# Optimization experiments

Measured on AMD Instinct MI355X. Metric: run time of the kernel, lower is better.

Reference implementation:

```python
import jax, jax.numpy as jnp
import numpy as np

EMBED_DIM = 1024
NUM_HEADS = 16
HEAD_DIM = EMBED_DIM // NUM_HEADS
SCALE = HEAD_DIM ** -0.5


def setup_inputs() -> dict:
    key = jax.random.key(0)
    k_x, k_qkv_w, k_qkv_b, k_p_w, k_p_b = jax.random.split(key, 5)
    B, N, C = 4, 2048, EMBED_DIM
    std = C ** -0.5
    return {
        "x": jax.random.normal(k_x, (B, N, C), dtype=jnp.float32),
        "qkv_w": jax.random.normal(k_qkv_w, (C, 3 * C), dtype=jnp.float32) * std,
        "qkv_b": jax.random.normal(k_qkv_b, (3 * C,), dtype=jnp.float32) * 0.02,
        "proj_w": jax.random.normal(k_p_w, (C, C), dtype=jnp.float32) * std,
        "proj_b": jax.random.normal(k_p_b, (C,), dtype=jnp.float32) * 0.02,
    }


def reference(x, qkv_w, qkv_b, proj_w, proj_b):
    B, N, C = x.shape
    H, D = NUM_HEADS, HEAD_DIM
    # fused QKV projection: [B, N, 3C] -> [3, B, H, N, D]
    qkv = (x @ qkv_w + qkv_b).reshape(B, N, 3, H, D).transpose(2, 0, 3, 1, 4)
    q, k, v = qkv[0], qkv[1], qkv[2]
    # explicit N x N attention (faithful to the original, no fused SDPA)
    attn = jnp.einsum("bhqd,bhkd->bhqk", q, k) * SCALE
    attn = jax.nn.softmax(attn, axis=-1)
    out = jnp.einsum("bhqk,bhkd->bhqd", attn, v)  # [B, H, N, D]
    out = out.transpose(0, 2, 1, 3).reshape(B, N, C)
    return out @ proj_w + proj_b
```

## Files before the change

kernel.cpp:

```cpp
#include <hip/hip_runtime.h>
#include <hip/hip_bf16.h>

typedef __bf16 bf16x8 __attribute__((ext_vector_type(8)));
typedef __bf16 bf16x4 __attribute__((ext_vector_type(4)));
typedef float  f32x4  __attribute__((ext_vector_type(4)));

#define MFMA_BF16(a, b, c) __builtin_amdgcn_mfma_f32_16x16x32_bf16((a), (b), (c), 0, 0, 0)

typedef const __attribute__((address_space(1))) void* gas_ptr;
typedef __attribute__((address_space(3))) void* las_ptr;

__device__ __forceinline__ void gload_lds16(const void* g, void* l) {
    __builtin_amdgcn_global_load_lds((gas_ptr)g, (las_ptr)l, 16, 0, 0);
}

__device__ __forceinline__ float fast_exp2(float x) {
#if __has_builtin(__builtin_amdgcn_exp2f)
    return __builtin_amdgcn_exp2f(x);
#else
    return __builtin_exp2f(x);
#endif
}

#define LOG2E 1.44269504088896f
#define QSCALE 0.1803368801111204f

__global__ __launch_bounds__(256) void prep_fused(const float* __restrict__ x,
                                                  const float* __restrict__ qkv_w,
                                                  const float* __restrict__ proj_w,
                                                  __bf16* __restrict__ Xb,
                                                  __bf16* __restrict__ Wqkvt,
                                                  __bf16* __restrict__ Wpt) {
    const int b = blockIdx.x;
    if (b < 8192) {
        int i = b * 256 + threadIdx.x;
        float4 v = ((const float4*)x)[i];
        bf16x4 o = {(__bf16)v.x, (__bf16)v.y, (__bf16)v.z, (__bf16)v.w};
        ((bf16x4*)Xb)[i] = o;
        return;
    }
    __shared__ float t[32][33];
    const float* in;
    __bf16* out;
    int R, C, bx, by;
    if (b < 11264) {
        int bb = b - 8192;
        in = qkv_w; out = Wqkvt; R = 1024; C = 3072;
        bx = (bb % 96) * 32; by = (bb / 96) * 32;
    } else {
        int bb = b - 11264;
        in = proj_w; out = Wpt; R = 1024; C = 1024;
        bx = (bb % 32) * 32; by = (bb / 32) * 32;
    }
    const int tx = threadIdx.x & 31, ty = threadIdx.x >> 5;
    int xcol = bx + tx;
    for (int j = ty; j < 32; j += 8)
        t[j][tx] = in[(size_t)(by + j) * C + xcol];
    __syncthreads();
    int x2 = by + tx;
    for (int j = ty; j < 32; j += 8)
        out[(size_t)(bx + j) * R + x2] = (__bf16)t[tx][j];
}

template <int MODE>
__global__ __launch_bounds__(256) void gemm_bt(const __bf16* __restrict__ A,
                                               const __bf16* __restrict__ Bt,
                                               const float* __restrict__ bias,
                                               float* __restrict__ outp,
                                               __bf16* __restrict__ Qp,
                                               __bf16* __restrict__ Kp,
                                               __bf16* __restrict__ Vp,
                                               int M, int Nn, int K) {
    __shared__ __align__(16) __bf16 SA[3][4096];
    __shared__ __align__(16) __bf16 SB[3][4096];
    const int tid = threadIdx.x, lane = tid & 63, w = tid >> 6;
    const int wr = w >> 1, wc = w & 1;
    const int nbx = Nn >> 7;
    const int nwg = (M >> 7) * nbx;
    const int cpx = nwg >> 3;
    const int id = blockIdx.x;
    const int nid = (id & 7) * cpx + (id >> 3);
    const int row0 = (nid / nbx) * 128, col0 = (nid % nbx) * 128;
    const __bf16* Ag = A + (size_t)row0 * K;
    const __bf16* Bg = Bt + (size_t)col0 * K;
    const int lr = lane >> 2;
    const int srcc = ((lane & 3) ^ ((lane >> 3) & 3)) * 8;
    const int frow = lane & 15, fq = lane >> 4;
    const int rdoff = (fq ^ ((frow >> 1) & 3)) * 8;
    f32x4 acc[4][4];
    for (int i = 0; i < 4; ++i)
        for (int j = 0; j < 4; ++j) acc[i][j] = (f32x4)0.f;

    auto stage = [&](int t, __bf16* Ad, __bf16* Bd) {
#pragma unroll
        for (int it = 0; it < 2; ++it) {
            int ci = 2 * w + it;
            gload_lds16(Ag + (size_t)(ci * 16 + lr) * K + t * 32 + srcc, Ad + ci * 512);
            gload_lds16(Bg + (size_t)(ci * 16 + lr) * K + t * 32 + srcc, Bd + ci * 512);
        }
    };

    const int NK = K >> 5;
    __bf16 *cA = SA[0], *cB = SB[0];
    __bf16 *nA = SA[1], *nB = SB[1];
    __bf16 *sA = SA[2], *sB = SB[2];
    stage(0, cA, cB);
    stage(1, nA, nB);

    for (int t = 0; t < NK; ++t) {
        if (t < NK - 1)
            asm volatile("s_waitcnt vmcnt(4)" ::: "memory");
        else
            asm volatile("s_waitcnt vmcnt(0)" ::: "memory");
        __builtin_amdgcn_s_barrier();
        if (t + 2 < NK) stage(t + 2, sA, sB);

        bf16x8 af[4], bf[4];
#pragma unroll
        for (int i = 0; i < 4; ++i)
            af[i] = *(const bf16x8*)&cA[(wr * 64 + i * 16 + frow) * 32 + rdoff];
#pragma unroll
        for (int j = 0; j < 4; ++j)
            bf[j] = *(const bf16x8*)&cB[(wc * 64 + j * 16 + frow) * 32 + rdoff];
#pragma unroll
        for (int i = 0; i < 4; ++i)
#pragma unroll
            for (int j = 0; j < 4; ++j) acc[i][j] = MFMA_BF16(af[i], bf[j], acc[i][j]);

        __bf16* tA = cA; cA = nA; nA = sA; sA = tA;
        __bf16* tB = cB; cB = nB; nB = sB; sB = tB;
    }

    for (int i = 0; i < 4; ++i) {
        int rbase = row0 + wr * 64 + i * 16 + fq * 4;
        for (int j = 0; j < 4; ++j) {
            int c = col0 + wc * 64 + j * 16 + frow;
            float bv = bias[c];
            if (MODE == 0) {
                int which = c >> 10;
                int h = (c >> 6) & 15;
                int d = c & 63;
                if (which == 2) {
                    int b = rbase >> 11, n = rbase & 2047;
                    int nph = (n & ~31) | (((n >> 2) & 3) << 3) | (((n >> 4) & 1) << 2) |
                              (n & 3);
                    bf16x4 vv = {(__bf16)(acc[i][j][0] + bv), (__bf16)(acc[i][j][1] + bv),
                                 (__bf16)(acc[i][j][2] + bv), (__bf16)(acc[i][j][3] + bv)};
                    *(bf16x4*)&Vp[(size_t)(((b << 4) + h) * 64 + d) * 2048 + nph] = vv;
                } else {
                    for (int rg = 0; rg < 4; ++rg) {
                        int rr = rbase + rg;
                        int b = rr >> 11, n = rr & 2047;
                        float v = acc[i][j][rg] + bv;
                        if (which == 0)
                            Qp[(size_t)(((b << 4) + h) * 2048 + n) * 64 + d] =
                                (__bf16)(v * QSCALE);
                        else
                            Kp[(size_t)(((b << 4) + h) * 2048 + n) * 64 + d] = (__bf16)v;
                    }
                }
            } else {
                for (int rg = 0; rg < 4; ++rg)
                    outp[(size_t)(rbase + rg) * Nn + c] = acc[i][j][rg] + bv;
            }
        }
    }
}

__global__ __launch_bounds__(256, 4) void flash_attn7(const __bf16* __restrict__ Q,
                                                      const __bf16* __restrict__ K,
                                                      const __bf16* __restrict__ Vt,
                                                      __bf16* __restrict__ O) {
    __shared__ __align__(16) __bf16 Kts[2][4096];
    __shared__ __align__(16) __bf16 Vts[2][4096];
    const int tid = threadIdx.x, lane = tid & 63, w = tid >> 6;
    const int frow = lane & 15, fq = lane >> 4;
    const int id = blockIdx.x;
    const int nid = (id & 7) * 128 + (id >> 3);
    const int bh = nid >> 4;
    const int q0 = (nid & 15) * 128;
    const __bf16* Qg = Q + ((size_t)bh * 2048 + q0 + w * 32) * 64;
    const __bf16* Kb = K + (size_t)bh * 2048 * 64;
    const __bf16* Vb = Vt + (size_t)bh * 64 * 2048;

    bf16x8 qf[2][2];
#pragma unroll
    for (int nt = 0; nt < 2; ++nt)
#pragma unroll
        for (int ks = 0; ks < 2; ++ks)
            qf[nt][ks] = *(const bf16x8*)(Qg + (nt * 16 + frow) * 64 + ks * 32 + fq * 8);

    bf16x8 ones;
#pragma unroll
    for (int i = 0; i < 8; ++i) ones[i] = (__bf16)1.0f;

    f32x4 acc[2][4];
#pragma unroll
    for (int i = 0; i < 2; ++i)
#pragma unroll
        for (int j = 0; j < 4; ++j) acc[i][j] = (f32x4)0.f;
    f32x4 acc_l[2];
#pragma unroll
    for (int i = 0; i < 2; ++i) acc_l[i] = (f32x4)0.f;

    const int s_r16 = lane >> 2;
    const int s_c8 = (((lane & 3) ^ ((lane >> 3) & 3))) * 8;

    auto stage = [&](int kt, __bf16* Kd, __bf16* Vd) {
#pragma unroll
        for (int it = 0; it < 2; ++it) {
            int ci = 2 * w + it;
            int ks = ci >> 2;
            int r16 = (ci & 3) * 16 + s_r16;
            gload_lds16(Kb + (size_t)(kt * 64 + r16) * 64 + ks * 32 + s_c8, Kd + ci * 512);
            gload_lds16(Vb + (size_t)r16 * 2048 + kt * 64 + ks * 32 + s_c8, Vd + ci * 512);
        }
    };

    stage(0, Kts[0], Vts[0]);

    const int key = (frow >> 1) & 3;
    const int slot = (fq ^ key) * 8;

    auto body = [&](int kt, const __bf16* Kc, const __bf16* Vc, __bf16* Kn, __bf16* Vn) {
        __syncthreads();
        if (kt < 31) stage(kt + 1, Kn, Vn);

#pragma unroll
        for (int ph = 0; ph < 2; ++ph) {
            bf16x8 pf[2];
#pragma unroll
            for (int mi = 0; mi < 2; ++mi) {
                int mt = ph * 2 + mi;
                bf16x8 a0 = *(const bf16x8*)&Kc[(mt * 16 + frow) * 32 + slot];
                bf16x8 a1 = *(const bf16x8*)&Kc[2048 + (mt * 16 + frow) * 32 + slot];
#pragma unroll
                for (int nt = 0; nt < 2; ++nt) {
                    f32x4 s = MFMA_BF16(a0, qf[nt][0], (f32x4)0.f);
                    s = MFMA_BF16(a1, qf[nt][1], s);
                    pf[nt][mi * 4 + 0] = (__bf16)fast_exp2(s[0]);
                    pf[nt][mi * 4 + 1] = (__bf16)fast_exp2(s[1]);
                    pf[nt][mi * 4 + 2] = (__bf16)fast_exp2(s[2]);
                    pf[nt][mi * 4 + 3] = (__bf16)fast_exp2(s[3]);
                }
            }

            __builtin_amdgcn_s_setprio(1);
#pragma unroll
            for (int nt = 0; nt < 4; ++nt) {
                bf16x8 vf = *(const bf16x8*)&Vc[ph * 2048 + (nt * 16 + frow) * 32 + slot];
                acc[0][nt] = MFMA_BF16(pf[0], vf, acc[0][nt]);
                acc[1][nt] = MFMA_BF16(pf[1], vf, acc[1][nt]);
            }
            acc_l[0] = MFMA_BF16(pf[0], ones, acc_l[0]);
            acc_l[1] = MFMA_BF16(pf[1], ones, acc_l[1]);
            __builtin_amdgcn_s_setprio(0);
        }
    };

    for (int kt = 0; kt < 32; kt += 2) {
        body(kt, Kts[0], Vts[0], Kts[1], Vts[1]);
        body(kt + 1, Kts[1], Vts[1], Kts[0], Vts[0]);
    }

    const int b = bh >> 4, h = bh & 15;
#pragma unroll
    for (int mq = 0; mq < 2; ++mq)
#pragma unroll
        for (int r = 0; r < 4; ++r) {
            float linv = 1.0f / acc_l[mq][r];
            int qg = q0 + w * 32 + mq * 16 + fq * 4 + r;
            __bf16* orow = O + ((size_t)(b * 2048 + qg)) * 1024 + h * 64 + frow;
#pragma unroll
            for (int nt = 0; nt < 4; ++nt)
                orow[nt * 16] = (__bf16)(acc[mq][nt][r] * linv);
        }
}

extern "C" void kernel_launch(void* const* d_in, const int* in_sizes, int n_in,
                              void* d_out, int out_size, void* d_ws, size_t ws_size,
                              hipStream_t stream) {
    const float* x      = (const float*)d_in[0];
    const float* qkv_w  = (const float*)d_in[1];
    const float* qkv_b  = (const float*)d_in[2];
    const float* proj_w = (const float*)d_in[3];
    const float* proj_b = (const float*)d_in[4];
    float* out = (float*)d_out;

    char* ws = (char*)d_ws;
    __bf16* Xb     = (__bf16*)(ws);
    __bf16* Wqkvt  = (__bf16*)(ws + 16777216);
    __bf16* Wpt    = (__bf16*)(ws + 23068672);
    __bf16* Qb     = (__bf16*)(ws + 25165824);
    __bf16* Kb     = (__bf16*)(ws + 41943040);
    __bf16* Vtb    = (__bf16*)(ws + 58720256);
    __bf16* AttnOut = Xb;

    prep_fused<<<12288, 256, 0, stream>>>(x, qkv_w, proj_w, Xb, Wqkvt, Wpt);

    gemm_bt<0><<<1536, 256, 0, stream>>>(Xb, Wqkvt, qkv_b, nullptr,
                                         Qb, Kb, Vtb, 8192, 3072, 1024);

    flash_attn7<<<1024, 256, 0, stream>>>(Qb, Kb, Vtb, AttnOut);

    gemm_bt<1><<<512, 256, 0, stream>>>(AttnOut, Wpt, proj_b, out,
                                        nullptr, nullptr, nullptr, 8192, 1024, 1024);
}
```

Measured before the change: 260.7 us.

## Replace QKV GEMM with 256x256-tile 8-wave kernel using interleaved LDS staging

Adds a new QKV projection GEMM that uses 256x256 output tiles with 512 threads (8 waves), 64-wide K steps, and a double-buffered LDS scheme. Global-to-LDS loads for the next tiles are interleaved with MFMA phases, and wave priority is raised around the math. Larger tiles raise arithmetic intensity and cut global traffic per FLOP. In exchange, LDS use and register pressure go up, and the grid shrinks to 384 workgroups, which may leave CUs underused or unbalanced.

```diff
diff --git a/kernel.cpp b/kernel.cpp
--- a/kernel.cpp
+++ b/kernel.cpp
@@ -60,6 +60,160 @@
     int x2 = by + tx;
     for (int j = ty; j < 32; j += 8)
         out[(size_t)(bx + j) * R + x2] = (__bf16)t[tx][j];
+}
+
+__global__ __launch_bounds__(512, 2) void gemm8_qkv(const __bf16* __restrict__ A,
+                                                    const __bf16* __restrict__ Bt,
+                                                    const float* __restrict__ bias,
+                                                    __bf16* __restrict__ Qp,
+                                                    __bf16* __restrict__ Kp,
+                                                    __bf16* __restrict__ Vp,
+                                                    int M, int Nn, int K) {
+    __shared__ __align__(16) __bf16 SA[2][2][8192];
+    __shared__ __align__(16) __bf16 SB[2][2][8192];
+    const int tid = threadIdx.x, lane = tid & 63, w = tid >> 6;
+    const int wr = w >> 2, wc = w & 3;
+    const int frow = lane & 15, fq = lane >> 4;
+    const int nbx = Nn >> 8;
+    const int nwg = (M >> 8) * nbx;
+    const int cpx = nwg >> 3;
+    const int id = blockIdx.x;
+    const int nid = (id & 7) * cpx + (id >> 3);
+    const int row0 = (nid / nbx) * 256, col0 = (nid % nbx) * 256;
+    const __bf16* Ag = A + (size_t)row0 * K;
+    const __bf16* Bg = Bt + (size_t)col0 * K;
+
+    const int srow = w * 8 + (lane >> 3);
+    const int csel8 = ((lane & 7) ^ ((lane >> 3) & 7)) * 8;
+    const int key = frow & 7;
+    const int sl0 = (fq ^ key) * 8;
+    const int sl1 = ((4 + fq) ^ key) * 8;
+    const int bro = (wc & 1) * 64;
+
+    const int NK = K >> 6;
+
+    f32x4 acc[8][4];
+#pragma unroll
+    for (int i = 0; i < 8; ++i)
+#pragma unroll
+        for (int j = 0; j < 4; ++j) acc[i][j] = (f32x4)0.f;
+    bf16x8 af[4][2];
+    bf16x8 bf[4][2];
+
+    auto stageA = [&](int tt, int ha, __bf16* dst) {
+#pragma unroll
+        for (int r = 0; r < 2; ++r)
+            gload_lds16(Ag + (size_t)(ha * 128 + r * 64 + srow) * K + tt * 64 + csel8,
+                        dst + r * 4096 + w * 512);
+    };
+    auto stageB = [&](int tt, int hb, __bf16* dst) {
+#pragma unroll
+        for (int r = 0; r < 2; ++r)
+            gload_lds16(Bg + (size_t)(hb * 128 + r * 64 + srow) * K + tt * 64 + csel8,
+                        dst + r * 4096 + w * 512);
+    };
+
+    stageB(0, 0, &SB[0][0][0]); stageB(0, 1, &SB[0][1][0]);
+    stageA(0, 0, &SA[0][0][0]); stageA(0, 1, &SA[0][1][0]);
+    stageB(1, 0, &SB[1][0][0]); stageB(1, 1, &SB[1][1][0]);
+    asm volatile("s_waitcnt vmcnt(4)" ::: "memory");
+    __builtin_amdgcn_s_barrier();
+
+    auto dsrA = [&](const __bf16* Ah, int q) {
+#pragma unroll
+        for (int i = 0; i < 4; ++i) {
+            const __bf16* rp = Ah + ((q * 4 + i) * 16 + frow) * 64;
+            af[i][0] = *(const bf16x8*)(rp + sl0);
+            af[i][1] = *(const bf16x8*)(rp + sl1);
+        }
+    };
+    auto dsrB = [&](const __bf16* Bh, int pr) {
+#pragma unroll
+        for (int n = 0; n < 2; ++n) {
+            const __bf16* rp = Bh + (bro + (pr * 2 + n) * 16 + frow) * 64;
+            bf[pr * 2 + n][0] = *(const bf16x8*)(rp + sl0);
+            bf[pr * 2 + n][1] = *(const bf16x8*)(rp + sl1);
+        }
+    };
+    auto mm = [&](int q, int pr) {
+        __builtin_amdgcn_s_setprio(1);
+#pragma unroll
+        for (int i = 0; i < 4; ++i)
+#pragma unroll
+            for (int n = 0; n < 2; ++n) {
+                acc[q * 4 + i][pr * 2 + n] =
+                    MFMA_BF16(af[i][0], bf[pr * 2 + n][0], acc[q * 4 + i][pr * 2 + n]);
+                acc[q * 4 + i][pr * 2 + n] =
+                    MFMA_BF16(af[i][1], bf[pr * 2 + n][1], acc[q * 4 + i][pr * 2 + n]);
+            }
+        __builtin_amdgcn_s_setprio(0);
+    };
+
+#define LGKM0 asm volatile("s_waitcnt lgkmcnt(0)" ::: "memory")
+#define BAR __builtin_amdgcn_s_barrier()
+
+    auto tile = [&](int t, __bf16* Ac0, __bf16* Ac1, __bf16* Bc0, __bf16* Bc1,
+                    __bf16* An0, __bf16* An1) {
+        const __bf16* Ah = (wr == 0) ? Ac0 : Ac1;
+        const __bf16* Bh = (wc < 2) ? Bc0 : Bc1;
+        dsrA(Ah, 0); dsrB(Bh, 0);
+        if (t + 1 < NK) stageA(t + 1, 0, An0);
+        BAR; LGKM0; mm(0, 0); BAR;
+        dsrB(Bh, 1);
+        if (t + 1 < NK) stageA(t + 1, 1, An1);
+        BAR; LGKM0; mm(0, 1); BAR;
+        dsrA(Ah, 1);
+        if (t + 2 < NK) stageB(t + 2, 0, Bc0);
+        BAR; LGKM0; mm(1, 1); BAR;
+        if (t + 2 < NK) stageB(t + 2, 1, Bc1);
+        BAR; mm(1, 0);
+        if (t + 1 < NK) {
+            if (t + 2 < NK)
+                asm volatile("s_waitcnt vmcnt(4)" ::: "memory");
+            else
+                asm volatile("s_waitcnt vmcnt(0)" ::: "memory");
+        }
+        BAR;
+    };
+
+    for (int t = 0; t < NK; t += 2) {
+        tile(t, &SA[0][0][0], &SA[0][1][0], &SB[0][0][0], &SB[0][1][0],
+             &SA[1][0][0], &SA[1][1][0]);
+        tile(t + 1, &SA[1][0][0], &SA[1][1][0], &SB[1][0][0], &SB[1][1][0],
+             &SA[0][0][0], &SA[0][1][0]);
+    }
+#undef LGKM0
+#undef BAR
+
+    for (int m = 0; m < 8; ++m) {
+        int rbase = row0 + wr * 128 + m * 16 + fq * 4;
+        for (int n = 0; n < 4; ++n) {
+            int c = col0 + wc * 64 + n * 16 + frow;
+            float bv = bias[c];
+            int which = c >> 10;
+            int h = (c >> 6) & 15;
+            int d = c & 63;
+            if (which == 2) {
+                int b = rbase >> 11, nn = rbase & 2047;
+                int nph = (nn & ~31) | (((nn >> 2) & 3) << 3) | (((nn >> 4) & 1) << 2) |
+                          (nn & 3);
+                bf16x4 vv = {(__bf16)(acc[m][n][0] + bv), (__bf16)(acc[m][n][1] + bv),
+                             (__bf16)(acc[m][n][2] + bv), (__bf16)(acc[m][n][3] + bv)};
+                *(bf16x4*)&Vp[(size_t)(((b << 4) + h) * 64 + d) * 2048 + nph] = vv;
+            } else {
+                for (int rg = 0; rg < 4; ++rg) {
+                    int rr = rbase + rg;
+                    int b = rr >> 11, nn = rr & 2047;
+                    float v = acc[m][n][rg] + bv;
+                    if (which == 0)
+                        Qp[(size_t)(((b << 4) + h) * 2048 + nn) * 64 + d] =
+                            (__bf16)(v * QSCALE);
+                    else
+                        Kp[(size_t)(((b << 4) + h) * 2048 + nn) * 64 + d] = (__bf16)v;
+                }
+            }
+        }
+    }
 }
 
 template <int MODE>
@@ -298,8 +452,7 @@
 
     prep_fused<<<12288, 256, 0, stream>>>(x, qkv_w, proj_w, Xb, Wqkvt, Wpt);
 
-    gemm_bt<0><<<1536, 256, 0, stream>>>(Xb, Wqkvt, qkv_b, nullptr,
-                                         Qb, Kb, Vtb, 8192, 3072, 1024);
+    gemm8_qkv<<<384, 512, 0, stream>>>(Xb, Wqkvt, qkv_b, Qb, Kb, Vtb, 8192, 3072, 1024);
 
     flash_attn7<<<1024, 256, 0, stream>>>(Qb, Kb, Vtb, AttnOut);
 
```

Result: no change. 265.2 us (+1.7%).
